# Kernel optimization log

Measured on AMD Instinct MI355X. Metric: run time of the kernel, lower is better.

## Reference

```python
import jax, jax.numpy as jnp
import numpy as np

NUM_ENTITIES = 100000
NUM_RELATIONS = 200          # 2*NUM_RELATIONS typed edges after adding inverses
DE = 200                     # entity embedding dim (= conv out channels)
DR = 200                     # relation embedding dim (in channels = DE+DR)
NUM_BASES = 4
N_NODES = 50000              # unique nodes in the extracted subgraph
N_TRIPLETS = 200000
N_EDGES = 2 * N_TRIPLETS     # forward + inverse edges


def setup_inputs() -> dict:
    key = jax.random.key(0)
    ks = jax.random.split(key, 10)
    # learned parameters
    entity_embedding = jax.random.normal(ks[0], (NUM_ENTITIES, DE), dtype=jnp.float32) * 0.05
    relation_embedding = jax.random.normal(ks[1], (NUM_RELATIONS, DR), dtype=jnp.float32) * 0.05
    # basis decomposition: W_r = sum_b att[r, b] * basis[b], basis: [B, in, out]
    xav = np.sqrt(2.0 / (DE + DR + DE)).astype(np.float32)
    basis = jax.random.normal(ks[2], (NUM_BASES, DE + DR, DE), dtype=jnp.float32) * xav
    att = jax.random.normal(ks[3], (2 * NUM_RELATIONS, NUM_BASES), dtype=jnp.float32) * 0.5
    # subgraph structure (precomputed numpy preprocessing from the torch forward)
    node_id = jax.random.randint(ks[4], (N_NODES,), 0, NUM_ENTITIES)
    src = jax.random.randint(ks[5], (N_TRIPLETS,), 0, N_NODES)
    dst = jax.random.randint(ks[6], (N_TRIPLETS,), 0, N_NODES)
    rel = jax.random.randint(ks[7], (N_TRIPLETS,), 0, NUM_RELATIONS)
    # doubling: (src->dst, rel) and inverse (dst->src, rel + NUM_RELATIONS);
    # rel_index (used to gather relation embeddings) stays un-shifted.
    edge_src = jnp.concatenate([src, dst])
    edge_dst = jnp.concatenate([dst, src])
    edge_type = jnp.concatenate([rel, rel + NUM_RELATIONS])
    rel_index = jnp.concatenate([rel, rel])
    return {
        "entity_embedding": entity_embedding,
        "relation_embedding": relation_embedding,
        "basis": basis,
        "att": att,
        "node_id": node_id,
        "edge_src": edge_src,
        "edge_dst": edge_dst,
        "edge_type": edge_type,
        "rel_index": rel_index,
        "unseen_index": 0,
    }


def reference(entity_embedding, relation_embedding, basis, att,
              node_id, edge_src, edge_dst, edge_type, rel_index, unseen_index):
    n_nodes = node_id.shape[0]
    # node features for the subgraph: [N, DE]
    x = entity_embedding[node_id]
    # per-edge relation embedding: [E, DR]
    rel = relation_embedding[rel_index]
    # message input: cat(source node emb, relation emb) -> [E, DE+DR]
    xj = jnp.concatenate([x[edge_src], rel], axis=1)
    # basis-decomposed relation-typed transform without materializing [E, in, out]:
    # project onto each basis first: [E, B, DE]
    h = jnp.einsum('ei,bio->ebo', xj, basis)
    # combine with relation-specific basis coefficients: [E, DE]
    msg = jnp.einsum('eb,ebo->eo', att[edge_type], h)
    # mean aggregation per destination node (edge_norm=None, root_weight/bias off)
    agg = jax.ops.segment_sum(msg, edge_dst, num_segments=n_nodes)
    cnt = jax.ops.segment_sum(jnp.ones(msg.shape[0], msg.dtype), edge_dst,
                              num_segments=n_nodes)
    embeddings = agg / jnp.maximum(cnt, 1.0)[:, None]
    # dropout is identity in eval mode
    return embeddings[unseen_index]
```

## Files before the change

kernel.cpp:

```cpp
#include <hip/hip_runtime.h>


#define DE 200
#define IN_DIM 400
#define NB 4
#define ROWS (NB * IN_DIM)
#define FBLOCKS 256
#define PBCAP 64
#define MAXE 128
#define CBLOCKS 50
#define CPB 4
#define KITER (ROWS / 64)

#define WS_CNT_OFF  0
#define WS_LIST_OFF 1024

__global__ __launch_bounds__(256)
void filter_k(const int4* __restrict__ edge_dst4,
              const int* __restrict__ edge_dst,
              const int* __restrict__ unseen,
              int n4, int n_edges,
              int* __restrict__ ws) {
    const int b = blockIdx.x;
    const int t = threadIdx.x;
    __shared__ int s_cnt;
    __shared__ int s_list[PBCAP];
    if (t == 0) s_cnt = 0;
    __syncthreads();

    const int u = unseen[0];
    for (int idx = b * blockDim.x + t; idx < n4; idx += FBLOCKS * blockDim.x) {
        const int4 v = edge_dst4[idx];
        const int  e = idx * 4;
        if (v.x == u) { int p = atomicAdd(&s_cnt, 1); if (p < PBCAP) s_list[p] = e;     }
        if (v.y == u) { int p = atomicAdd(&s_cnt, 1); if (p < PBCAP) s_list[p] = e + 1; }
        if (v.z == u) { int p = atomicAdd(&s_cnt, 1); if (p < PBCAP) s_list[p] = e + 2; }
        if (v.w == u) { int p = atomicAdd(&s_cnt, 1); if (p < PBCAP) s_list[p] = e + 3; }
    }
    if (b == 0 && t < (n_edges & 3)) {
        const int e = n4 * 4 + t;
        if (edge_dst[e] == u) { int p = atomicAdd(&s_cnt, 1); if (p < PBCAP) s_list[p] = e; }
    }
    __syncthreads();
    if (t == 0) ws[WS_CNT_OFF + b] = s_cnt;
    const int cl = s_cnt < PBCAP ? s_cnt : PBCAP;
    if (t < cl) ws[WS_LIST_OFF + b * PBCAP + t] = s_list[t];
}

__global__ __launch_bounds__(256)
void compute_k(const float* __restrict__ Eemb,
               const float* __restrict__ Remb,
               const float* __restrict__ basis,
               const float* __restrict__ att,
               const int* __restrict__ node_id,
               const int* __restrict__ edge_src,
               const int* __restrict__ edge_type,
               const int* __restrict__ rel_index,
               const int* __restrict__ ws,
               float* __restrict__ out) {
    const int t  = threadIdx.x;
    const int c  = t & 3;
    const int rg = t >> 2;
    const int o  = blockIdx.x * CPB + c;

    float rv[KITER];
    #pragma unroll
    for (int k = 0; k < KITER; ++k)
        rv[k] = basis[(size_t)(rg + 64 * k) * DE + o];

    __shared__ int   s_counts[FBLOCKS];
    __shared__ unsigned long long s_mask[FBLOCKS / 64];
    __shared__ int   s_edges[MAXE];
    __shared__ int   s_srcrow[MAXE];
    __shared__ int   s_ri[MAXE];
    __shared__ float s_att[MAXE][NB];
    __shared__ int   s_total, s_listed;
    __shared__ float s_y[ROWS];
    __shared__ float s_part[256];

    const int cv = ws[WS_CNT_OFF + t];
    s_counts[t] = cv;
    const unsigned long long bal = __ballot(cv > 0);
    if ((t & 63) == 0) s_mask[t >> 6] = bal;
    __syncthreads();
    if (t == 0) {
        int tot = 0, listed = 0;
        for (int w = 0; w < FBLOCKS / 64; ++w) {
            unsigned long long m = s_mask[w];
            while (m) {
                const int bb = w * 64 + __builtin_ctzll(m);
                m &= m - 1;
                const int cb = s_counts[bb];
                tot += cb;
                const int cl = cb < PBCAP ? cb : PBCAP;
                for (int k = 0; k < cl && listed < MAXE; ++k)
                    s_edges[listed++] = ws[WS_LIST_OFF + bb * PBCAP + k];
            }
        }
        s_total  = tot;
        s_listed = listed;
    }
    __syncthreads();
    const int cnt = s_listed;

    if (t < cnt) {
        const int e = s_edges[t];
        s_srcrow[t] = node_id[edge_src[e]];
        s_ri[t]     = rel_index[e];
        const int typ = edge_type[e];
        #pragma unroll
        for (int b = 0; b < NB; ++b) s_att[t][b] = att[typ * NB + b];
    }
    __syncthreads();

    for (int i = t; i < IN_DIM; i += 256) {
        float y0 = 0.f, y1 = 0.f, y2 = 0.f, y3 = 0.f;
        for (int j = 0; j < cnt; ++j) {
            const float xv = (i < DE)
                ? Eemb[(size_t)s_srcrow[j] * DE + i]
                : Remb[(size_t)s_ri[j] * DE + (i - DE)];
            y0 += s_att[j][0] * xv;
            y1 += s_att[j][1] * xv;
            y2 += s_att[j][2] * xv;
            y3 += s_att[j][3] * xv;
        }
        s_y[0 * IN_DIM + i] = y0;
        s_y[1 * IN_DIM + i] = y1;
        s_y[2 * IN_DIM + i] = y2;
        s_y[3 * IN_DIM + i] = y3;
    }
    __syncthreads();

    float acc = 0.f;
    #pragma unroll
    for (int k = 0; k < KITER; ++k)
        acc += rv[k] * s_y[rg + 64 * k];

    s_part[t] = acc;
    __syncthreads();
    #pragma unroll
    for (int off = 128; off >= 4; off >>= 1) {
        if (t < off) s_part[t] += s_part[t + off];
        __syncthreads();
    }
    if (t < CPB) {
        int cd = s_total;
        if (cd < 1) cd = 1;
        out[blockIdx.x * CPB + t] = s_part[t] / (float)cd;
    }
}

extern "C" void kernel_launch(void* const* d_in, const int* in_sizes, int n_in,
                              void* d_out, int out_size, void* d_ws, size_t ws_size,
                              hipStream_t stream) {
    const float* Eemb  = (const float*)d_in[0];
    const float* Remb  = (const float*)d_in[1];
    const float* basis = (const float*)d_in[2];
    const float* att   = (const float*)d_in[3];
    const int* node_id  = (const int*)d_in[4];
    const int* edge_src = (const int*)d_in[5];
    const int* edge_dst = (const int*)d_in[6];
    const int* edge_typ = (const int*)d_in[7];
    const int* rel_idx  = (const int*)d_in[8];
    const int* unseen   = (const int*)d_in[9];
    float* out = (float*)d_out;
    int*   ws  = (int*)d_ws;

    const int n_edges = in_sizes[6];
    const int n4 = n_edges / 4;

    filter_k<<<FBLOCKS, 256, 0, stream>>>((const int4*)edge_dst, edge_dst,
                                          unseen, n4, n_edges, ws);

    compute_k<<<CBLOCKS, 256, 0, stream>>>(Eemb, Remb, basis, att, node_id,
                                           edge_src, edge_typ, rel_idx,
                                           ws, out);
}
```

Baseline: 131.9 us.

## Fuse edge filter and compute into a single redundant-scan kernel

Merges the two-kernel pipeline into one launch where each of 25 blocks of 1024 threads redundantly scans edge_dst for the target node, removing the workspace round-trip and second launch. The final reduction uses wave shuffles plus a small shared array instead of a tree of syncthreads. In exchange every block rereads the whole edge_dst array with far fewer CUs participating in the scan, and the listed-edge cap drops to 64.

```diff
diff --git a/kernel.cpp b/kernel.cpp
--- a/kernel.cpp
+++ b/kernel.cpp
@@ -5,106 +5,72 @@
 #define IN_DIM 400
 #define NB 4
 #define ROWS (NB * IN_DIM)
-#define FBLOCKS 256
+#define CBLOCKS 25
+#define CPB 8
+#define NTHR 1024
+#define RG (NTHR / CPB)
+#define KITER ((ROWS + RG - 1) / RG)
+#define NWAVES (NTHR / 64)
 #define PBCAP 64
-#define MAXE 128
-#define CBLOCKS 50
-#define CPB 4
-#define KITER (ROWS / 64)
 
-#define WS_CNT_OFF  0
-#define WS_LIST_OFF 1024
+__global__ __launch_bounds__(NTHR, 4)
+void fused_k(const float* __restrict__ Eemb,
+             const float* __restrict__ Remb,
+             const float* __restrict__ basis,
+             const float* __restrict__ att,
+             const int* __restrict__ node_id,
+             const int* __restrict__ edge_src,
+             const int* __restrict__ edge_dst,
+             const int* __restrict__ edge_type,
+             const int* __restrict__ rel_index,
+             const int* __restrict__ unseen,
+             int n_edges,
+             float* __restrict__ out)
+{
+    const int t  = threadIdx.x;
+    const int c  = t & (CPB - 1);
+    const int rg = t >> 3;
+    const int o  = blockIdx.x * CPB + c;
 
-__global__ __launch_bounds__(256)
-void filter_k(const int4* __restrict__ edge_dst4,
-              const int* __restrict__ edge_dst,
-              const int* __restrict__ unseen,
-              int n4, int n_edges,
-              int* __restrict__ ws) {
-    const int b = blockIdx.x;
-    const int t = threadIdx.x;
-    __shared__ int s_cnt;
-    __shared__ int s_list[PBCAP];
+    float rv[KITER];
+    #pragma unroll
+    for (int k = 0; k < KITER; ++k) {
+        const int row = rg + RG * k;
+        rv[k] = (row < ROWS) ? basis[(size_t)row * DE + o] : 0.f;
+    }
+
+    __shared__ int   s_cnt;
+    __shared__ int   s_list[PBCAP];
+    __shared__ int   s_srcrow[PBCAP];
+    __shared__ int   s_ri[PBCAP];
+    __shared__ float s_att[PBCAP][NB];
+    __shared__ float s_y[ROWS];
+    __shared__ float s_wp[NWAVES * CPB];
+
     if (t == 0) s_cnt = 0;
     __syncthreads();
 
-    const int u = unseen[0];
-    for (int idx = b * blockDim.x + t; idx < n4; idx += FBLOCKS * blockDim.x) {
-        const int4 v = edge_dst4[idx];
+    const int u  = unseen[0];
+    const int n4 = n_edges >> 2;
+    const int4* ed4 = (const int4*)edge_dst;
+    for (int idx = t; idx < n4; idx += NTHR) {
+        const int4 v = ed4[idx];
         const int  e = idx * 4;
         if (v.x == u) { int p = atomicAdd(&s_cnt, 1); if (p < PBCAP) s_list[p] = e;     }
         if (v.y == u) { int p = atomicAdd(&s_cnt, 1); if (p < PBCAP) s_list[p] = e + 1; }
         if (v.z == u) { int p = atomicAdd(&s_cnt, 1); if (p < PBCAP) s_list[p] = e + 2; }
         if (v.w == u) { int p = atomicAdd(&s_cnt, 1); if (p < PBCAP) s_list[p] = e + 3; }
     }
-    if (b == 0 && t < (n_edges & 3)) {
+    if (t < (n_edges & 3)) {
         const int e = n4 * 4 + t;
         if (edge_dst[e] == u) { int p = atomicAdd(&s_cnt, 1); if (p < PBCAP) s_list[p] = e; }
     }
     __syncthreads();
-    if (t == 0) ws[WS_CNT_OFF + b] = s_cnt;
-    const int cl = s_cnt < PBCAP ? s_cnt : PBCAP;
-    if (t < cl) ws[WS_LIST_OFF + b * PBCAP + t] = s_list[t];
-}
-
-__global__ __launch_bounds__(256)
-void compute_k(const float* __restrict__ Eemb,
-               const float* __restrict__ Remb,
-               const float* __restrict__ basis,
-               const float* __restrict__ att,
-               const int* __restrict__ node_id,
-               const int* __restrict__ edge_src,
-               const int* __restrict__ edge_type,
-               const int* __restrict__ rel_index,
-               const int* __restrict__ ws,
-               float* __restrict__ out) {
-    const int t  = threadIdx.x;
-    const int c  = t & 3;
-    const int rg = t >> 2;
-    const int o  = blockIdx.x * CPB + c;
-
-    float rv[KITER];
-    #pragma unroll
-    for (int k = 0; k < KITER; ++k)
-        rv[k] = basis[(size_t)(rg + 64 * k) * DE + o];
-
-    __shared__ int   s_counts[FBLOCKS];
-    __shared__ unsigned long long s_mask[FBLOCKS / 64];
-    __shared__ int   s_edges[MAXE];
-    __shared__ int   s_srcrow[MAXE];
-    __shared__ int   s_ri[MAXE];
-    __shared__ float s_att[MAXE][NB];
-    __shared__ int   s_total, s_listed;
-    __shared__ float s_y[ROWS];
-    __shared__ float s_part[256];
-
-    const int cv = ws[WS_CNT_OFF + t];
-    s_counts[t] = cv;
-    const unsigned long long bal = __ballot(cv > 0);
-    if ((t & 63) == 0) s_mask[t >> 6] = bal;
-    __syncthreads();
-    if (t == 0) {
-        int tot = 0, listed = 0;
-        for (int w = 0; w < FBLOCKS / 64; ++w) {
-            unsigned long long m = s_mask[w];
-            while (m) {
-                const int bb = w * 64 + __builtin_ctzll(m);
-                m &= m - 1;
-                const int cb = s_counts[bb];
-                tot += cb;
-                const int cl = cb < PBCAP ? cb : PBCAP;
-                for (int k = 0; k < cl && listed < MAXE; ++k)
-                    s_edges[listed++] = ws[WS_LIST_OFF + bb * PBCAP + k];
-            }
-        }
-        s_total  = tot;
-        s_listed = listed;
-    }
-    __syncthreads();
-    const int cnt = s_listed;
+    const int cnt_true = s_cnt;
+    const int cnt = cnt_true < PBCAP ? cnt_true : PBCAP;
 
     if (t < cnt) {
-        const int e = s_edges[t];
+        const int e = s_list[t];
         s_srcrow[t] = node_id[edge_src[e]];
         s_ri[t]     = rel_index[e];
         const int typ = edge_type[e];
@@ -113,40 +79,44 @@
     }
     __syncthreads();
 
-    for (int i = t; i < IN_DIM; i += 256) {
+    if (t < IN_DIM) {
         float y0 = 0.f, y1 = 0.f, y2 = 0.f, y3 = 0.f;
         for (int j = 0; j < cnt; ++j) {
-            const float xv = (i < DE)
-                ? Eemb[(size_t)s_srcrow[j] * DE + i]
-                : Remb[(size_t)s_ri[j] * DE + (i - DE)];
+            const float xv = (t < DE)
+                ? Eemb[(size_t)s_srcrow[j] * DE + t]
+                : Remb[(size_t)s_ri[j] * DE + (t - DE)];
             y0 += s_att[j][0] * xv;
             y1 += s_att[j][1] * xv;
             y2 += s_att[j][2] * xv;
             y3 += s_att[j][3] * xv;
         }
-        s_y[0 * IN_DIM + i] = y0;
-        s_y[1 * IN_DIM + i] = y1;
-        s_y[2 * IN_DIM + i] = y2;
-        s_y[3 * IN_DIM + i] = y3;
+        s_y[0 * IN_DIM + t] = y0;
+        s_y[1 * IN_DIM + t] = y1;
+        s_y[2 * IN_DIM + t] = y2;
+        s_y[3 * IN_DIM + t] = y3;
     }
     __syncthreads();
 
     float acc = 0.f;
     #pragma unroll
-    for (int k = 0; k < KITER; ++k)
-        acc += rv[k] * s_y[rg + 64 * k];
+    for (int k = 0; k < KITER; ++k) {
+        const int row = rg + RG * k;
+        if (row < ROWS) acc += rv[k] * s_y[row];
+    }
 
-    s_part[t] = acc;
+    acc += __shfl_xor(acc, 32);
+    acc += __shfl_xor(acc, 16);
+    acc += __shfl_xor(acc, 8);
+    const int wave = t >> 6;
+    if ((t & 63) < CPB) s_wp[wave * CPB + (t & 63)] = acc;
     __syncthreads();
-    #pragma unroll
-    for (int off = 128; off >= 4; off >>= 1) {
-        if (t < off) s_part[t] += s_part[t + off];
-        __syncthreads();
-    }
+
     if (t < CPB) {
-        int cd = s_total;
-        if (cd < 1) cd = 1;
-        out[blockIdx.x * CPB + t] = s_part[t] / (float)cd;
+        float s = 0.f;
+        #pragma unroll
+        for (int w = 0; w < NWAVES; ++w) s += s_wp[w * CPB + t];
+        int cd = cnt_true < 1 ? 1 : cnt_true;
+        out[blockIdx.x * CPB + t] = s / (float)cd;
     }
 }
 
@@ -164,15 +134,10 @@
     const int* rel_idx  = (const int*)d_in[8];
     const int* unseen   = (const int*)d_in[9];
     float* out = (float*)d_out;
-    int*   ws  = (int*)d_ws;
 
     const int n_edges = in_sizes[6];
-    const int n4 = n_edges / 4;
 
-    filter_k<<<FBLOCKS, 256, 0, stream>>>((const int4*)edge_dst, edge_dst,
-                                          unseen, n4, n_edges, ws);
-
-    compute_k<<<CBLOCKS, 256, 0, stream>>>(Eemb, Remb, basis, att, node_id,
-                                           edge_src, edge_typ, rel_idx,
-                                           ws, out);
+    fused_k<<<CBLOCKS, NTHR, 0, stream>>>(Eemb, Remb, basis, att, node_id,
+                                          edge_src, edge_dst, edge_typ,
+                                          rel_idx, unseen, n_edges, out);
 }
```

Measured after the change: 161.3 us. +22.2%, slower.
